# Kernel tuning notes

Hardware: AMD Instinct MI355X
Metric: run time of the kernel (lower is better)

The kernel has to match this reference:

```python
import jax, jax.numpy as jnp
import numpy as np
from math import sqrt

ALPHA = 1.0
EPS = 1e-8


def setup_inputs() -> dict:
    key = jax.random.key(0)
    k1, k2, k3 = jax.random.split(key, 3)
    B, L, S, H, E = 4, 2048, 2048, 8, 64
    queries = jax.random.normal(k1, (B, L, H, E), dtype=jnp.float32)
    keys = jax.random.normal(k2, (B, S, H, E), dtype=jnp.float32)
    values = jax.random.normal(k3, (B, S, H, E), dtype=jnp.float32)
    return {"queries": queries, "keys": keys, "values": values}


def reference(queries, keys, values):
    B, L, H, E = queries.shape
    scale = 1.0 / sqrt(E)
    # [B,H,L,S] dot-product scores
    dot_product = jnp.einsum('blhe,bshe->bhls', queries, keys)
    # squared norms: [B,H,L,1] and [B,H,1,S]
    queries_norm2 = jnp.sum(queries * queries, axis=-1).transpose(0, 2, 1)[..., None]
    keys_norm2 = jnp.sum(keys * keys, axis=-1).transpose(0, 2, 1)[..., None, :]
    # wedge (exterior product) norm: |q|^2|k|^2 - (q.k)^2, clamped at 0
    wedge_norm2 = jax.nn.relu(queries_norm2 * keys_norm2 - dot_product * dot_product)
    wedge_norm = jnp.sqrt(wedge_norm2 + EPS)
    scores = ((1.0 - ALPHA) * dot_product + ALPHA * wedge_norm) * scale
    A = jax.nn.softmax(scores, axis=-1)  # dropout p=0 (eval)
    V = jnp.einsum('bhls,bshd->blhd', A, values)
    return V, jnp.mean(jnp.abs(scores))
```

## Files before the change

### kernel.cpp

```cpp
#include <hip/hip_runtime.h>
#include <hip/hip_bf16.h>


#define B_ 4
#define L_ 2048
#define S_ 2048
#define H_ 8
#define E_ 64
#define EPS_ 1e-8f
#define SC2_ 0.18033688011112042f
#define LN2_ 0.6931471805599453f
#define LDP 72
#define ROWSTR (H_ * E_)

#define K_OFF 0
#define V_OFF 8388608
#define KN_OFF 16777216
#define SS_OFF 17039360
#define WS_NEED 17039364

typedef __attribute__((ext_vector_type(8))) short bf16x8;
typedef __attribute__((ext_vector_type(4))) short bf16x4v;
typedef __attribute__((ext_vector_type(4))) float f32x4;

union bfr8 { bf16x8 v; unsigned u[4]; };

static __device__ __forceinline__ unsigned pk2(float lo, float hi) {
  union { __hip_bfloat162 h2; unsigned u; } cv;
  cv.h2 = __float22bfloat162_rn(float2{lo, hi});
  return cv.u;
}
static __device__ __forceinline__ short f2bf_rne(float x) {
  union { float f; unsigned u; } v; v.f = x;
  unsigned r = (v.u + 0x7FFF + ((v.u >> 16) & 1)) >> 16;
  return (short)(unsigned short)r;
}
static __device__ __forceinline__ float bf2f(short h) {
  union { unsigned u; float f; } v; v.u = ((unsigned)(unsigned short)h) << 16;
  return v.f;
}
static __device__ __forceinline__ float fast_sqrt(float x) {
  float r; asm("v_sqrt_f32 %0, %1" : "=v"(r) : "v"(x)); return r;
}
static __device__ __forceinline__ float fast_exp2(float x) {
  float r; asm("v_exp_f32 %0, %1" : "=v"(r) : "v"(x)); return r;
}
static __device__ __forceinline__ void gload16(const void* g, void* l) {
  __builtin_amdgcn_global_load_lds((const __attribute__((address_space(1))) void*)g,
                                   (__attribute__((address_space(3))) void*)l, 16, 0, 0);
}

__global__ void prep_kv(const float* __restrict__ K, const float* __restrict__ V,
                        short* __restrict__ Kg, short* __restrict__ Vg,
                        float* __restrict__ kn2g) {
  __shared__ __align__(16) short TT[64 * 80];
  const int tid = threadIdx.x;
  const int raw = blockIdx.x;
  const bool isK = raw < 1024;
  const int bidx = isK ? raw : raw - 1024;
  const int st = bidx & 31;
  const int bh = bidx >> 5;
  const int b = bh >> 3, h = bh & 7;
  const size_t src_base = (size_t)b * (L_ * ROWSTR) + (size_t)(st * 64) * ROWSTR + (size_t)h * E_;

  if (isK) {
    short* dst = Kg + (size_t)bidx * 4096;
    const int s = tid >> 2;
    float part = 0.f;
#pragma unroll
    for (int q = 0; q < 2; ++q) {
      const int ch = (2 * tid + q) & 7;
      const int esrc = (ch ^ (s & 7)) * 8;
      const float* sp = K + src_base + (size_t)s * ROWSTR + esrc;
      const float4 a = *reinterpret_cast<const float4*>(sp);
      const float4 c4 = *reinterpret_cast<const float4*>(sp + 4);
      part += a.x*a.x + a.y*a.y + a.z*a.z + a.w*a.w
            + c4.x*c4.x + c4.y*c4.y + c4.z*c4.z + c4.w*c4.w;
      bfr8 o;
      o.u[0] = pk2(a.x, a.y);  o.u[1] = pk2(a.z, a.w);
      o.u[2] = pk2(c4.x, c4.y); o.u[3] = pk2(c4.z, c4.w);
      *reinterpret_cast<bf16x8*>(dst + s * 64 + ch * 8) = o.v;
    }
    part += __shfl_xor(part, 1);
    part += __shfl_xor(part, 2);
    if ((tid & 3) == 0) kn2g[(size_t)bidx * 64 + s] = part;
  } else {
    short* dst = Vg + (size_t)bidx * 4096;
    {
      const int s = tid >> 2;
      const int e0 = (tid & 3) * 16;
      const float* sp = V + src_base + (size_t)s * ROWSTR + e0;
      const float4 a0 = *reinterpret_cast<const float4*>(sp);
      const float4 a1 = *reinterpret_cast<const float4*>(sp + 4);
      const float4 a2 = *reinterpret_cast<const float4*>(sp + 8);
      const float4 a3 = *reinterpret_cast<const float4*>(sp + 12);
      bfr8 t0, t1;
      t0.u[0] = pk2(a0.x, a0.y); t0.u[1] = pk2(a0.z, a0.w);
      t0.u[2] = pk2(a1.x, a1.y); t0.u[3] = pk2(a1.z, a1.w);
      t1.u[0] = pk2(a2.x, a2.y); t1.u[1] = pk2(a2.z, a2.w);
      t1.u[2] = pk2(a3.x, a3.y); t1.u[3] = pk2(a3.z, a3.w);
      *reinterpret_cast<bf16x8*>(&TT[s * 80 + e0]) = t0.v;
      *reinterpret_cast<bf16x8*>(&TT[s * 80 + e0 + 8]) = t1.v;
    }
    __syncthreads();
    const int e = tid >> 2;
#pragma unroll
    for (int q = 0; q < 2; ++q) {
      const int ch = (2 * tid + q) & 7;
      const int s0 = (ch ^ (e & 7)) * 8;
      bfr8 o;
#pragma unroll
      for (int j = 0; j < 4; ++j) {
        const unsigned lo = (unsigned short)TT[(s0 + 2 * j) * 80 + e];
        const unsigned hi = (unsigned short)TT[(s0 + 2 * j + 1) * 80 + e];
        o.u[j] = lo | (hi << 16);
      }
      *reinterpret_cast<bf16x8*>(dst + e * 64 + ch * 8) = o.v;
    }
  }
}

__launch_bounds__(256, 4)
__global__ void geom_attn(const float* __restrict__ Q,
                          const short* __restrict__ Kg,
                          const short* __restrict__ Vg,
                          const float* __restrict__ kn2g,
                          float* __restrict__ out,
                          float* __restrict__ ssum_g) {
  __shared__ __align__(16) short Kl[2][4096];
  __shared__ __align__(16) short Vl[4096];
  __shared__ __align__(16) short Plds[4][16 * LDP];

  const int tid = threadIdx.x;
  const int lane = tid & 63;
  const int w = tid >> 6;
  const int g = lane >> 4;
  const int c = lane & 15;
  const int cx = c & 7;

  const int vbk = ((blockIdx.x & 7) << 7) + (blockIdx.x >> 3);
  const int qt = vbk & 31;
  const int bh = vbk >> 5;
  const int b = bh >> 3, h = bh & 7;
  const int q0 = qt * 64;

  const size_t qbase = (size_t)b * (L_ * ROWSTR) + (size_t)h * E_;

  bfr8 qa[2];
  float qn2row[4];
  {
    const int qrow = q0 + w * 16 + c;
    const float* qp = Q + qbase + (size_t)qrow * ROWSTR;
    float qs = 0.f;
#pragma unroll
    for (int ch = 0; ch < 2; ++ch) {
      const float4 a = *reinterpret_cast<const float4*>(qp + ch * 32 + g * 8);
      const float4 b4 = *reinterpret_cast<const float4*>(qp + ch * 32 + g * 8 + 4);
      qa[ch].u[0] = pk2(a.x, a.y);  qa[ch].u[1] = pk2(a.z, a.w);
      qa[ch].u[2] = pk2(b4.x, b4.y); qa[ch].u[3] = pk2(b4.z, b4.w);
      qs += a.x*a.x + a.y*a.y + a.z*a.z + a.w*a.w
          + b4.x*b4.x + b4.y*b4.y + b4.z*b4.z + b4.w*b4.w;
    }
    qs += __shfl_xor(qs, 16);
    qs += __shfl_xor(qs, 32);
#pragma unroll
    for (int i = 0; i < 4; ++i) qn2row[i] = __shfl(qs, g * 4 + i);
  }

  float lsum[4] = {0.f, 0.f, 0.f, 0.f};
  f32x4 o[4];
#pragma unroll
  for (int dt = 0; dt < 4; ++dt) o[dt] = (f32x4){0.f, 0.f, 0.f, 0.f};
  float ssum = 0.f;

  const char* Ksrc = (const char*)(Kg + (size_t)(bh * 32) * 4096);
  const char* Vsrc = (const char*)(Vg + (size_t)(bh * 32) * 4096);
  const float* knb = kn2g + (size_t)(bh * 32) * 64;

  const int wb = w * 2048;

  float kn_cur[4], kn_next[4];
#pragma unroll
  for (int sub = 0; sub < 4; ++sub) kn_cur[sub] = knb[sub * 16 + c];

  gload16(Ksrc + wb + lane * 16,        (char*)&Kl[0][0] + wb);
  gload16(Ksrc + wb + 1024 + lane * 16, (char*)&Kl[0][0] + wb + 1024);

  for (int kt = 0; kt < 32; ++kt) {
    const int cb = kt & 1;
    const int nx = (kt + 1) & 31;
    __syncthreads();

#pragma unroll
    for (int sub = 0; sub < 4; ++sub) kn_next[sub] = knb[nx * 64 + sub * 16 + c];
    __builtin_amdgcn_sched_barrier(0);
    const char* vs = Vsrc + (size_t)kt * 8192;
    gload16(vs + wb + lane * 16,        (char*)&Vl[0] + wb);
    gload16(vs + wb + 1024 + lane * 16, (char*)&Vl[0] + wb + 1024);
    const char* ks = Ksrc + (size_t)nx * 8192;
    gload16(ks + wb + lane * 16,        (char*)&Kl[cb ^ 1][0] + wb);
    gload16(ks + wb + 1024 + lane * 16, (char*)&Kl[cb ^ 1][0] + wb + 1024);

#pragma unroll
    for (int sub = 0; sub < 4; ++sub) {
      const int s = sub * 16 + c;
      f32x4 acc = (f32x4){0.f, 0.f, 0.f, 0.f};
#pragma unroll
      for (int ch = 0; ch < 2; ++ch) {
        const int idx = s * 64 + (((ch * 4 + g) ^ cx) << 3);
        const bf16x8 bh8 = *reinterpret_cast<const bf16x8*>(&Kl[cb][idx]);
        acc = __builtin_amdgcn_mfma_f32_16x16x32_bf16(qa[ch].v, bh8, acc, 0, 0, 0);
      }
#pragma unroll
      for (int i = 0; i < 4; ++i) {
        const float dot = acc[i];
        const float w2 = fmaxf(fmaf(-dot, dot, qn2row[i] * kn_cur[sub]), EPS_);
        const float s2 = SC2_ * fast_sqrt(w2);
        ssum += s2;
        const float p = fast_exp2(s2);
        union { float f; unsigned u; } pu; pu.f = p;
        union { unsigned u; float f; } pt; pt.u = pu.u & 0xffff0000u;
        lsum[i] += pt.f;
        Plds[w][(g * 4 + i) * LDP + s] = (short)(unsigned short)(pu.u >> 16);
      }
    }

    asm volatile("s_waitcnt vmcnt(2)\n\ts_barrier" ::: "memory");

#pragma unroll
    for (int ks2 = 0; ks2 < 2; ++ks2) {
      const bf16x8 pa = *reinterpret_cast<const bf16x8*>(&Plds[w][c * LDP + ks2 * 32 + g * 8]);
#pragma unroll
      for (int dt = 0; dt < 4; ++dt) {
        const int er = dt * 16 + c;
        const int idx = er * 64 + (((ks2 * 4 + g) ^ cx) << 3);
        const bf16x8 vb8 = *reinterpret_cast<const bf16x8*>(&Vl[idx]);
        o[dt] = __builtin_amdgcn_mfma_f32_16x16x32_bf16(pa, vb8, o[dt], 0, 0, 0);
      }
    }
#pragma unroll
    for (int sub = 0; sub < 4; ++sub) kn_cur[sub] = kn_next[sub];
  }

#pragma unroll
  for (int m = 1; m < 16; m <<= 1)
#pragma unroll
    for (int i = 0; i < 4; ++i) lsum[i] += __shfl_xor(lsum[i], m);

#pragma unroll
  for (int i = 0; i < 4; ++i) {
    const float inv = 1.0f / lsum[i];
    const int qrow = q0 + w * 16 + g * 4 + i;
    float* op = out + (size_t)b * (L_ * ROWSTR) + (size_t)qrow * ROWSTR + (size_t)h * E_;
#pragma unroll
    for (int dt = 0; dt < 4; ++dt)
      op[dt * 16 + c] = o[dt][i] * inv;
  }

#pragma unroll
  for (int m = 1; m < 64; m <<= 1) ssum += __shfl_xor(ssum, m);
  if (lane == 0) atomicAdd(ssum_g, ssum);
}

__global__ void geom_fin(const float* __restrict__ ws, float* __restrict__ out) {
  out[(size_t)B_ * L_ * H_ * E_] = ws[0] * (LN2_ / 134217728.0f);
}

__launch_bounds__(256, 2)
__global__ void geom_attn_v1(const float* __restrict__ Q, const float* __restrict__ K,
                             const float* __restrict__ V, float* __restrict__ out,
                             float* __restrict__ score_sum) {
  __shared__ __align__(16) short Khi[64 * LDP];
  __shared__ __align__(16) short Klo[64 * LDP];
  __shared__ __align__(16) short Vt[64 * LDP];
  __shared__ __align__(16) short Plds[4][16 * LDP];
  __shared__ float kn2[64];
  __shared__ float qn2[64];

  const int tid = threadIdx.x;
  const int lane = tid & 63;
  const int w = tid >> 6;
  const int g = lane >> 4;
  const int c = lane & 15;
  const int bidx = blockIdx.x;
  const int qt = bidx & 31;
  const int h = (bidx >> 5) & 7;
  const int b = bidx >> 8;
  const int q0 = qt * 64;
  const size_t bh_base = (size_t)b * L_ * ROWSTR + (size_t)h * E_;

  bf16x8 qhi[2], qlo[2];
  {
    const int qrow = q0 + w * 16 + c;
    const float* qp = Q + bh_base + (size_t)qrow * ROWSTR;
    float qs = 0.f;
#pragma unroll
    for (int ch = 0; ch < 2; ++ch) {
      const float4 a = *reinterpret_cast<const float4*>(qp + ch * 32 + g * 8);
      const float4 bq = *reinterpret_cast<const float4*>(qp + ch * 32 + g * 8 + 4);
      const float xs[8] = {a.x,a.y,a.z,a.w,bq.x,bq.y,bq.z,bq.w};
#pragma unroll
      for (int j = 0; j < 8; ++j) {
        const float x = xs[j];
        qs += x * x;
        const short hs = f2bf_rne(x);
        qhi[ch][j] = hs;
        qlo[ch][j] = f2bf_rne(x - bf2f(hs));
      }
    }
    qs += __shfl_xor(qs, 16);
    qs += __shfl_xor(qs, 32);
    if (lane < 16) qn2[w * 16 + c] = qs;
  }
  __syncthreads();
  float qn2row[4];
#pragma unroll
  for (int i = 0; i < 4; ++i) qn2row[i] = qn2[w * 16 + g * 4 + i];

  float m_i[4] = {0,0,0,0}, lsum[4] = {0,0,0,0};
  f32x4 o[4];
#pragma unroll
  for (int dt = 0; dt < 4; ++dt) o[dt] = (f32x4){0,0,0,0};
  float ssum = 0.f;

  for (int kt = 0; kt < S_ / 64; ++kt) {
    __syncthreads();
    {
      const int r0 = tid >> 4, c4 = tid & 15;
      const size_t kbase = bh_base + (size_t)(kt * 64) * ROWSTR + c4 * 4;
      float part[4];
#pragma unroll
      for (int i = 0; i < 4; ++i) {
        const int r = r0 + 16 * i;
        const float4 kv = *reinterpret_cast<const float4*>(K + kbase + (size_t)r * ROWSTR);
        part[i] = kv.x*kv.x + kv.y*kv.y + kv.z*kv.z + kv.w*kv.w;
        const short h0 = f2bf_rne(kv.x), h1 = f2bf_rne(kv.y), h2 = f2bf_rne(kv.z), h3 = f2bf_rne(kv.w);
        bf16x4v hv = {h0, h1, h2, h3};
        *reinterpret_cast<bf16x4v*>(&Khi[r * LDP + c4 * 4]) = hv;
        bf16x4v lv = {f2bf_rne(kv.x - bf2f(h0)), f2bf_rne(kv.y - bf2f(h1)),
                      f2bf_rne(kv.z - bf2f(h2)), f2bf_rne(kv.w - bf2f(h3))};
        *reinterpret_cast<bf16x4v*>(&Klo[r * LDP + c4 * 4]) = lv;
        const float4 vv = *reinterpret_cast<const float4*>(V + kbase + (size_t)r * ROWSTR);
        Vt[(c4 * 4 + 0) * LDP + r] = f2bf_rne(vv.x);
        Vt[(c4 * 4 + 1) * LDP + r] = f2bf_rne(vv.y);
        Vt[(c4 * 4 + 2) * LDP + r] = f2bf_rne(vv.z);
        Vt[(c4 * 4 + 3) * LDP + r] = f2bf_rne(vv.w);
      }
#pragma unroll
      for (int m = 1; m < 16; m <<= 1)
#pragma unroll
        for (int i = 0; i < 4; ++i) part[i] += __shfl_xor(part[i], m);
      if (c4 < 4) kn2[r0 + 16 * c4] = part[c4];
    }
    __syncthreads();

    float sv[4][4];
    float tm[4] = {0,0,0,0};
#pragma unroll
    for (int sub = 0; sub < 4; ++sub) {
      const int s = sub * 16 + c;
      f32x4 acc = (f32x4){0,0,0,0};
#pragma unroll
      for (int ch = 0; ch < 2; ++ch) {
        const int e = ch * 32 + g * 8;
        const bf16x8 bh8 = *reinterpret_cast<const bf16x8*>(&Khi[s * LDP + e]);
        const bf16x8 bl8 = *reinterpret_cast<const bf16x8*>(&Klo[s * LDP + e]);
        acc = __builtin_amdgcn_mfma_f32_16x16x32_bf16(qhi[ch], bh8, acc, 0, 0, 0);
        acc = __builtin_amdgcn_mfma_f32_16x16x32_bf16(qlo[ch], bh8, acc, 0, 0, 0);
        acc = __builtin_amdgcn_mfma_f32_16x16x32_bf16(qhi[ch], bl8, acc, 0, 0, 0);
      }
      const float kn = kn2[s];
#pragma unroll
      for (int i = 0; i < 4; ++i) {
        const float dot = acc[i];
        float w2 = fmaxf(qn2row[i] * kn - dot * dot, 0.f) + EPS_;
        const float sc = 0.125f * sqrtf(w2);
        sv[sub][i] = sc;
        tm[i] = fmaxf(tm[i], sc);
        ssum += sc;
      }
    }
#pragma unroll
    for (int m = 1; m < 16; m <<= 1)
#pragma unroll
      for (int i = 0; i < 4; ++i) tm[i] = fmaxf(tm[i], __shfl_xor(tm[i], m));
    float r_[4];
#pragma unroll
    for (int i = 0; i < 4; ++i) {
      const float mn = fmaxf(m_i[i], tm[i]);
      r_[i] = __expf(m_i[i] - mn);
      m_i[i] = mn;
      lsum[i] *= r_[i];
    }
#pragma unroll
    for (int dt = 0; dt < 4; ++dt)
#pragma unroll
      for (int i = 0; i < 4; ++i) o[dt][i] *= r_[i];
#pragma unroll
    for (int sub = 0; sub < 4; ++sub) {
      const int s = sub * 16 + c;
#pragma unroll
      for (int i = 0; i < 4; ++i) {
        const float p = __expf(sv[sub][i] - m_i[i]);
        lsum[i] += p;
        Plds[w][(g * 4 + i) * LDP + s] = f2bf_rne(p);
      }
    }
    __syncthreads();
#pragma unroll
    for (int ks = 0; ks < 2; ++ks) {
      const bf16x8 pa = *reinterpret_cast<const bf16x8*>(&Plds[w][c * LDP + ks * 32 + g * 8]);
#pragma unroll
      for (int dt = 0; dt < 4; ++dt) {
        const bf16x8 vb8 = *reinterpret_cast<const bf16x8*>(&Vt[(dt * 16 + c) * LDP + ks * 32 + g * 8]);
        o[dt] = __builtin_amdgcn_mfma_f32_16x16x32_bf16(pa, vb8, o[dt], 0, 0, 0);
      }
    }
  }
#pragma unroll
  for (int m = 1; m < 16; m <<= 1)
#pragma unroll
    for (int i = 0; i < 4; ++i) lsum[i] += __shfl_xor(lsum[i], m);
#pragma unroll
  for (int i = 0; i < 4; ++i) {
    const float inv = 1.0f / lsum[i];
    const int qrow = q0 + w * 16 + g * 4 + i;
    float* op = out + (size_t)b * L_ * ROWSTR + (size_t)qrow * ROWSTR + (size_t)h * E_;
#pragma unroll
    for (int dt = 0; dt < 4; ++dt) op[dt * 16 + c] = o[dt][i] * inv;
  }
#pragma unroll
  for (int m = 1; m < 64; m <<= 1) ssum += __shfl_xor(ssum, m);
  if (lane == 0) atomicAdd(score_sum, ssum);
}

__global__ void geom_fin_v1(const float* __restrict__ ws, float* __restrict__ out) {
  out[(size_t)B_ * L_ * H_ * E_] = ws[0] * (1.0f / 134217728.0f);
}

extern "C" void kernel_launch(void* const* d_in, const int* in_sizes, int n_in,
                              void* d_out, int out_size, void* d_ws, size_t ws_size,
                              hipStream_t stream) {
  const float* Q = (const float*)d_in[0];
  const float* K = (const float*)d_in[1];
  const float* V = (const float*)d_in[2];
  float* out = (float*)d_out;

  if (ws_size >= (size_t)WS_NEED) {
    short* Kg = (short*)((char*)d_ws + K_OFF);
    short* Vg = (short*)((char*)d_ws + V_OFF);
    float* kn2g = (float*)((char*)d_ws + KN_OFF);
    float* ss = (float*)((char*)d_ws + SS_OFF);
    hipMemsetAsync(ss, 0, sizeof(float), stream);
    prep_kv<<<dim3(2048), dim3(256), 0, stream>>>(K, V, Kg, Vg, kn2g);
    geom_attn<<<dim3(1024), dim3(256), 0, stream>>>(Q, Kg, Vg, kn2g, out, ss);
    geom_fin<<<dim3(1), dim3(1), 0, stream>>>(ss, out);
  } else {
    float* ss = (float*)d_ws;
    hipMemsetAsync(ss, 0, sizeof(float), stream);
    geom_attn_v1<<<dim3(1024), dim3(256), 0, stream>>>(Q, K, V, out, ss);
    geom_fin_v1<<<dim3(1), dim3(1), 0, stream>>>(ss, out);
  }
}
```

Baseline: 193.8 us.

## Use 128-row query tiles with 8 waves, double-buffer V, transpose QK MFMA

The attention kernel now runs 512-thread blocks over 128-query tiles, so each staged K/V tile is shared by twice as many rows. V is double-buffered alongside K, which removes the mid-iteration vmcnt barrier. The QK MFMA operands are swapped so each lane holds four keys for one query, which lets P be packed with v_cvt_pk_bf16_f32 into a single 8-byte LDS store. The V prep is rewritten to transpose through strided global loads instead of an LDS staging buffer. In exchange the kernel uses more LDS per block and launches half as many blocks, which may lower occupancy.

```diff
diff --git a/kernel.cpp b/kernel.cpp
--- a/kernel.cpp
+++ b/kernel.cpp
@@ -30,6 +30,11 @@
   cv.h2 = __float22bfloat162_rn(float2{lo, hi});
   return cv.u;
 }
+static __device__ __forceinline__ unsigned cvtpk(float lo, float hi) {
+  unsigned r;
+  asm("v_cvt_pk_bf16_f32 %0, %1, %2" : "=v"(r) : "v"(lo), "v"(hi));
+  return r;
+}
 static __device__ __forceinline__ short f2bf_rne(float x) {
   union { float f; unsigned u; } v; v.f = x;
   unsigned r = (v.u + 0x7FFF + ((v.u >> 16) & 1)) >> 16;
@@ -53,7 +58,6 @@
 __global__ void prep_kv(const float* __restrict__ K, const float* __restrict__ V,
                         short* __restrict__ Kg, short* __restrict__ Vg,
                         float* __restrict__ kn2g) {
-  __shared__ __align__(16) short TT[64 * 80];
   const int tid = threadIdx.x;
   const int raw = blockIdx.x;
   const bool isK = raw < 1024;
@@ -86,41 +90,29 @@
     if ((tid & 3) == 0) kn2g[(size_t)bidx * 64 + s] = part;
   } else {
     short* dst = Vg + (size_t)bidx * 4096;
-    {
-      const int s = tid >> 2;
-      const int e0 = (tid & 3) * 16;
-      const float* sp = V + src_base + (size_t)s * ROWSTR + e0;
-      const float4 a0 = *reinterpret_cast<const float4*>(sp);
-      const float4 a1 = *reinterpret_cast<const float4*>(sp + 4);
-      const float4 a2 = *reinterpret_cast<const float4*>(sp + 8);
-      const float4 a3 = *reinterpret_cast<const float4*>(sp + 12);
-      bfr8 t0, t1;
-      t0.u[0] = pk2(a0.x, a0.y); t0.u[1] = pk2(a0.z, a0.w);
-      t0.u[2] = pk2(a1.x, a1.y); t0.u[3] = pk2(a1.z, a1.w);
-      t1.u[0] = pk2(a2.x, a2.y); t1.u[1] = pk2(a2.z, a2.w);
-      t1.u[2] = pk2(a3.x, a3.y); t1.u[3] = pk2(a3.z, a3.w);
-      *reinterpret_cast<bf16x8*>(&TT[s * 80 + e0]) = t0.v;
-      *reinterpret_cast<bf16x8*>(&TT[s * 80 + e0 + 8]) = t1.v;
-    }
-    __syncthreads();
-    const int e = tid >> 2;
+    const int e = tid & 63;
+    const int sc0 = tid >> 6;
 #pragma unroll
     for (int q = 0; q < 2; ++q) {
-      const int ch = (2 * tid + q) & 7;
-      const int s0 = (ch ^ (e & 7)) * 8;
+      const int sc = sc0 + q * 4;
+      const float* sp = V + src_base + (size_t)(sc * 8) * ROWSTR + e;
+      float v0 = sp[0];
+      float v1 = sp[1 * ROWSTR];
+      float v2 = sp[2 * ROWSTR];
+      float v3 = sp[3 * ROWSTR];
+      float v4 = sp[4 * ROWSTR];
+      float v5 = sp[5 * ROWSTR];
+      float v6 = sp[6 * ROWSTR];
+      float v7 = sp[7 * ROWSTR];
       bfr8 o;
-#pragma unroll
-      for (int j = 0; j < 4; ++j) {
-        const unsigned lo = (unsigned short)TT[(s0 + 2 * j) * 80 + e];
-        const unsigned hi = (unsigned short)TT[(s0 + 2 * j + 1) * 80 + e];
-        o.u[j] = lo | (hi << 16);
-      }
-      *reinterpret_cast<bf16x8*>(dst + e * 64 + ch * 8) = o.v;
-    }
-  }
-}
-
-__launch_bounds__(256, 4)
+      o.u[0] = pk2(v0, v1); o.u[1] = pk2(v2, v3);
+      o.u[2] = pk2(v4, v5); o.u[3] = pk2(v6, v7);
+      *reinterpret_cast<bf16x8*>(dst + e * 64 + ((sc ^ (e & 7)) * 8)) = o.v;
+    }
+  }
+}
+
+__launch_bounds__(512, 4)
 __global__ void geom_attn(const float* __restrict__ Q,
                           const short* __restrict__ Kg,
                           const short* __restrict__ Vg,
@@ -128,8 +120,8 @@
                           float* __restrict__ out,
                           float* __restrict__ ssum_g) {
   __shared__ __align__(16) short Kl[2][4096];
-  __shared__ __align__(16) short Vl[4096];
-  __shared__ __align__(16) short Plds[4][16 * LDP];
+  __shared__ __align__(16) short Vl[2][4096];
+  __shared__ __align__(16) short Plds[8][16 * LDP];
 
   const int tid = threadIdx.x;
   const int lane = tid & 63;
@@ -138,16 +130,16 @@
   const int c = lane & 15;
   const int cx = c & 7;
 
-  const int vbk = ((blockIdx.x & 7) << 7) + (blockIdx.x >> 3);
-  const int qt = vbk & 31;
-  const int bh = vbk >> 5;
+  const int vbk = ((blockIdx.x & 7) << 6) + (blockIdx.x >> 3);
+  const int qt = vbk & 15;
+  const int bh = vbk >> 4;
   const int b = bh >> 3, h = bh & 7;
-  const int q0 = qt * 64;
+  const int q0 = qt * 128;
 
   const size_t qbase = (size_t)b * (L_ * ROWSTR) + (size_t)h * E_;
 
   bfr8 qa[2];
-  float qn2row[4];
+  float qn2sc;
   {
     const int qrow = q0 + w * 16 + c;
     const float* qp = Q + qbase + (size_t)qrow * ROWSTR;
@@ -163,93 +155,90 @@
     }
     qs += __shfl_xor(qs, 16);
     qs += __shfl_xor(qs, 32);
-#pragma unroll
-    for (int i = 0; i < 4; ++i) qn2row[i] = __shfl(qs, g * 4 + i);
-  }
-
-  float lsum[4] = {0.f, 0.f, 0.f, 0.f};
+    qn2sc = qs;
+  }
+
+  float lsum4[4] = {0.f, 0.f, 0.f, 0.f};
+  float ssum4[4] = {0.f, 0.f, 0.f, 0.f};
   f32x4 o[4];
 #pragma unroll
   for (int dt = 0; dt < 4; ++dt) o[dt] = (f32x4){0.f, 0.f, 0.f, 0.f};
-  float ssum = 0.f;
 
   const char* Ksrc = (const char*)(Kg + (size_t)(bh * 32) * 4096);
   const char* Vsrc = (const char*)(Vg + (size_t)(bh * 32) * 4096);
   const float* knb = kn2g + (size_t)(bh * 32) * 64;
 
-  const int wb = w * 2048;
-
-  float kn_cur[4], kn_next[4];
-#pragma unroll
-  for (int sub = 0; sub < 4; ++sub) kn_cur[sub] = knb[sub * 16 + c];
-
-  gload16(Ksrc + wb + lane * 16,        (char*)&Kl[0][0] + wb);
-  gload16(Ksrc + wb + 1024 + lane * 16, (char*)&Kl[0][0] + wb + 1024);
+  float4 kn_cur[4], kn_nx[4];
+#pragma unroll
+  for (int sub = 0; sub < 4; ++sub)
+    kn_cur[sub] = *reinterpret_cast<const float4*>(knb + sub * 16 + g * 4);
+
+  gload16(Ksrc + w * 1024 + lane * 16, (char*)&Kl[0][0] + w * 1024);
+  gload16(Vsrc + w * 1024 + lane * 16, (char*)&Vl[0][0] + w * 1024);
 
   for (int kt = 0; kt < 32; ++kt) {
     const int cb = kt & 1;
-    const int nx = (kt + 1) & 31;
     __syncthreads();
 
-#pragma unroll
-    for (int sub = 0; sub < 4; ++sub) kn_next[sub] = knb[nx * 64 + sub * 16 + c];
-    __builtin_amdgcn_sched_barrier(0);
-    const char* vs = Vsrc + (size_t)kt * 8192;
-    gload16(vs + wb + lane * 16,        (char*)&Vl[0] + wb);
-    gload16(vs + wb + 1024 + lane * 16, (char*)&Vl[0] + wb + 1024);
-    const char* ks = Ksrc + (size_t)nx * 8192;
-    gload16(ks + wb + lane * 16,        (char*)&Kl[cb ^ 1][0] + wb);
-    gload16(ks + wb + 1024 + lane * 16, (char*)&Kl[cb ^ 1][0] + wb + 1024);
+    if (kt + 1 < 32) {
+      const int nx = kt + 1;
+#pragma unroll
+      for (int sub = 0; sub < 4; ++sub)
+        kn_nx[sub] = *reinterpret_cast<const float4*>(knb + nx * 64 + sub * 16 + g * 4);
+      __builtin_amdgcn_sched_barrier(0);
+      gload16(Ksrc + (size_t)nx * 8192 + w * 1024 + lane * 16, (char*)&Kl[cb ^ 1][0] + w * 1024);
+      gload16(Vsrc + (size_t)nx * 8192 + w * 1024 + lane * 16, (char*)&Vl[cb ^ 1][0] + w * 1024);
+    }
 
 #pragma unroll
     for (int sub = 0; sub < 4; ++sub) {
-      const int s = sub * 16 + c;
       f32x4 acc = (f32x4){0.f, 0.f, 0.f, 0.f};
 #pragma unroll
       for (int ch = 0; ch < 2; ++ch) {
-        const int idx = s * 64 + (((ch * 4 + g) ^ cx) << 3);
-        const bf16x8 bh8 = *reinterpret_cast<const bf16x8*>(&Kl[cb][idx]);
-        acc = __builtin_amdgcn_mfma_f32_16x16x32_bf16(qa[ch].v, bh8, acc, 0, 0, 0);
-      }
+        const int idx = (sub * 16 + c) * 64 + (((ch * 4 + g) ^ cx) << 3);
+        const bf16x8 kh8 = *reinterpret_cast<const bf16x8*>(&Kl[cb][idx]);
+        acc = __builtin_amdgcn_mfma_f32_16x16x32_bf16(kh8, qa[ch].v, acc, 0, 0, 0);
+      }
+      const float4 kn = kn_cur[sub];
+      float p[4];
 #pragma unroll
       for (int i = 0; i < 4; ++i) {
         const float dot = acc[i];
-        const float w2 = fmaxf(fmaf(-dot, dot, qn2row[i] * kn_cur[sub]), EPS_);
+        const float knv = (i == 0) ? kn.x : (i == 1) ? kn.y : (i == 2) ? kn.z : kn.w;
+        const float w2 = fmaxf(fmaf(-dot, dot, fmaf(qn2sc, knv, EPS_)), EPS_);
         const float s2 = SC2_ * fast_sqrt(w2);
-        ssum += s2;
-        const float p = fast_exp2(s2);
-        union { float f; unsigned u; } pu; pu.f = p;
-        union { unsigned u; float f; } pt; pt.u = pu.u & 0xffff0000u;
-        lsum[i] += pt.f;
-        Plds[w][(g * 4 + i) * LDP + s] = (short)(unsigned short)(pu.u >> 16);
-      }
-    }
-
-    asm volatile("s_waitcnt vmcnt(2)\n\ts_barrier" ::: "memory");
-
-#pragma unroll
-    for (int ks2 = 0; ks2 < 2; ++ks2) {
-      const bf16x8 pa = *reinterpret_cast<const bf16x8*>(&Plds[w][c * LDP + ks2 * 32 + g * 8]);
+        ssum4[i] += s2;
+        p[i] = fast_exp2(s2);
+        lsum4[i] += p[i];
+      }
+      uint2 pw;
+      pw.x = cvtpk(p[0], p[1]);
+      pw.y = cvtpk(p[2], p[3]);
+      *reinterpret_cast<uint2*>(&Plds[w][c * LDP + sub * 16 + g * 4]) = pw;
+    }
+
+#pragma unroll
+    for (int ks = 0; ks < 2; ++ks) {
+      const bf16x8 pa = *reinterpret_cast<const bf16x8*>(&Plds[w][c * LDP + ks * 32 + g * 8]);
 #pragma unroll
       for (int dt = 0; dt < 4; ++dt) {
-        const int er = dt * 16 + c;
-        const int idx = er * 64 + (((ks2 * 4 + g) ^ cx) << 3);
-        const bf16x8 vb8 = *reinterpret_cast<const bf16x8*>(&Vl[idx]);
+        const int idx = (dt * 16 + c) * 64 + (((ks * 4 + g) ^ cx) << 3);
+        const bf16x8 vb8 = *reinterpret_cast<const bf16x8*>(&Vl[cb][idx]);
         o[dt] = __builtin_amdgcn_mfma_f32_16x16x32_bf16(pa, vb8, o[dt], 0, 0, 0);
       }
     }
 #pragma unroll
-    for (int sub = 0; sub < 4; ++sub) kn_cur[sub] = kn_next[sub];
-  }
-
-#pragma unroll
-  for (int m = 1; m < 16; m <<= 1)
-#pragma unroll
-    for (int i = 0; i < 4; ++i) lsum[i] += __shfl_xor(lsum[i], m);
+    for (int sub = 0; sub < 4; ++sub) kn_cur[sub] = kn_nx[sub];
+  }
+
+  float lsum = (lsum4[0] + lsum4[1]) + (lsum4[2] + lsum4[3]);
+  lsum += __shfl_xor(lsum, 16);
+  lsum += __shfl_xor(lsum, 32);
+  const float rinv = 1.0f / lsum;
 
 #pragma unroll
   for (int i = 0; i < 4; ++i) {
-    const float inv = 1.0f / lsum[i];
+    const float inv = __shfl(rinv, g * 4 + i);
     const int qrow = q0 + w * 16 + g * 4 + i;
     float* op = out + (size_t)b * (L_ * ROWSTR) + (size_t)qrow * ROWSTR + (size_t)h * E_;
 #pragma unroll
@@ -257,6 +246,7 @@
       op[dt * 16 + c] = o[dt][i] * inv;
   }
 
+  float ssum = (ssum4[0] + ssum4[1]) + (ssum4[2] + ssum4[3]);
 #pragma unroll
   for (int m = 1; m < 64; m <<= 1) ssum += __shfl_xor(ssum, m);
   if (lane == 0) atomicAdd(ssum_g, ssum);
@@ -453,7 +443,7 @@
     float* ss = (float*)((char*)d_ws + SS_OFF);
     hipMemsetAsync(ss, 0, sizeof(float), stream);
     prep_kv<<<dim3(2048), dim3(256), 0, stream>>>(K, V, Kg, Vg, kn2g);
-    geom_attn<<<dim3(1024), dim3(256), 0, stream>>>(Q, Kg, Vg, kn2g, out, ss);
+    geom_attn<<<dim3(512), dim3(512), 0, stream>>>(Q, Kg, Vg, kn2g, out, ss);
     geom_fin<<<dim3(1), dim3(1), 0, stream>>>(ss, out);
   } else {
     float* ss = (float*)d_ws;
```

Result: slower. 199.2 us (+2.8%).
